# Kernel tuning notes

Hardware: AMD Instinct MI355X
Metric: run time of the kernel (lower is better)

Reference implementation:

```python
import jax, jax.numpy as jnp
import numpy as np

B, S, HID = 4, 2048, 576
NH, NKV, HD = 9, 3, 64
MAXPOS, THETA = 8192, 100000.0


def rotate_half(x):
    x1, x2 = x[..., : x.shape[-1] // 2], x[..., x.shape[-1] // 2 :]
    return jnp.concatenate((-x2, x1), axis=-1)


def setup_inputs() -> dict:
    key = jax.random.key(0)
    ks = jax.random.split(key, 6)
    x = jax.random.normal(ks[0], (B, S, HID), dtype=jnp.float32)
    # RoPE tables (HuggingFace layout: freqs duplicated across halves)
    inv_freq = 1.0 / (THETA ** (np.arange(0, HD, 2, dtype=np.float32) / HD))
    freqs = np.outer(np.arange(MAXPOS, dtype=np.float32), inv_freq)
    emb = np.concatenate([freqs, freqs], axis=-1)
    cos = jnp.asarray(np.cos(emb))
    sin = jnp.asarray(np.sin(emb))
    position_ids = jnp.broadcast_to(jnp.arange(S, dtype=jnp.int64), (B, S))
    # additive causal mask [B,1,S,S]
    causal = jnp.where(
        jnp.tril(jnp.ones((S, S), dtype=bool)), 0.0, -1e9
    ).astype(jnp.float32)
    attention_mask = jnp.broadcast_to(causal, (B, 1, S, S))
    scale = 0.02
    wq = jax.random.normal(ks[1], (NH * HD, HID), dtype=jnp.float32) * scale
    wk = jax.random.normal(ks[2], (NKV * HD, HID), dtype=jnp.float32) * scale
    wv = jax.random.normal(ks[3], (NKV * HD, HID), dtype=jnp.float32) * scale
    wo = jax.random.normal(ks[4], (HID, NH * HD), dtype=jnp.float32) * scale
    return {
        "x": x, "cos": cos, "sin": sin, "position_ids": position_ids,
        "attention_mask": attention_mask,
        "wq": wq, "wk": wk, "wv": wv, "wo": wo,
    }


def reference(x, cos, sin, position_ids, attention_mask, wq, wk, wv, wo):
    b, s, _ = x.shape
    # projections (nn.Linear: y = x @ W.T), split into heads -> [B,H,S,D]
    q = (x @ wq.T).reshape(b, s, NH, HD).transpose(0, 2, 1, 3)
    k = (x @ wk.T).reshape(b, s, NKV, HD).transpose(0, 2, 1, 3)
    v = (x @ wv.T).reshape(b, s, NKV, HD).transpose(0, 2, 1, 3)
    # RoPE: cos/sin gathered per position -> [B,1,S,D], broadcast over heads
    c = cos[position_ids][:, None, :, :]
    si = sin[position_ids][:, None, :, :]
    q = q * c + rotate_half(q) * si
    k = k * c + rotate_half(k) * si
    # GQA expansion: repeat_interleave kv heads to match q heads
    k = jnp.repeat(k, NH // NKV, axis=1)
    v = jnp.repeat(v, NH // NKV, axis=1)
    scale = 1.0 / jnp.sqrt(jnp.asarray(HD, dtype=x.dtype))
    scores = jnp.einsum("bhqd,bhkd->bhqk", q, k) * scale + attention_mask
    attn = jax.nn.softmax(scores.astype(jnp.float32), axis=-1).astype(q.dtype)
    out = jnp.einsum("bhqk,bhkd->bhqd", attn, v)
    out = out.transpose(0, 2, 1, 3).reshape(b, s, NH * HD)
    return out @ wo.T
```

## Files before the change

### kernel.cpp

```cpp
#include <hip/hip_runtime.h>
#include <hip/hip_bf16.h>

#define B_    4
#define S_    2048
#define HID_  576
#define NH_   9
#define NKV_  3
#define HD_   64
#define GQ_   3

typedef __attribute__((ext_vector_type(8))) short bf16x8;
typedef __attribute__((ext_vector_type(4))) float f32x4;

__device__ __forceinline__ short f2bf(float f) {
    union { float f; unsigned int u; } v; v.f = f;
    unsigned int r = (v.u + 0x7fffu + ((v.u >> 16) & 1u)) >> 16;
    return (short)r;
}

__device__ __forceinline__ float exp2fast(float x) {
    return __builtin_amdgcn_exp2f(x);
}

__device__ __forceinline__ void async16(const void* g, void* l) {
    __builtin_amdgcn_global_load_lds(
        (const __attribute__((address_space(1))) unsigned int*)g,
        (__attribute__((address_space(3))) unsigned int*)l, 16, 0, 0);
}

#define NX_   (8192 * 576)
#define NWQ_  (576 * 576)
#define NWK_  (192 * 576)
#define NWV_  (192 * 576)
#define NWO_  (576 * 576)
#define NTOT_ (NX_ + NWQ_ + NWK_ + NWV_ + NWO_)

__global__ __launch_bounds__(256) void convert_kernel(
    const float* __restrict__ x,  const float* __restrict__ wq,
    const float* __restrict__ wk, const float* __restrict__ wv,
    const float* __restrict__ wo,
    short* __restrict__ xb, short* __restrict__ wqkvb, short* __restrict__ wob)
{
    int i4 = (blockIdx.x * 256 + threadIdx.x) * 4;
    const float* src; short* dst;
    if (i4 < NX_)                          { src = x  + i4;                          dst = xb    + i4; }
    else if (i4 < NX_ + NWQ_)              { src = wq + (i4 - NX_);                  dst = wqkvb + (i4 - NX_); }
    else if (i4 < NX_ + NWQ_ + NWK_)       { src = wk + (i4 - NX_ - NWQ_);           dst = wqkvb + (i4 - NX_); }
    else if (i4 < NX_ + NWQ_ + NWK_ + NWV_){ src = wv + (i4 - NX_ - NWQ_ - NWK_);    dst = wqkvb + (i4 - NX_); }
    else                                   { src = wo + (i4 - NX_ - NWQ_ - NWK_ - NWV_);
                                             dst = wob + (i4 - NX_ - NWQ_ - NWK_ - NWV_); }
    float4 v = *(const float4*)src;
    short4 o = make_short4(f2bf(v.x), f2bf(v.y), f2bf(v.z), f2bf(v.w));
    *(short4*)dst = o;
}

__global__ __launch_bounds__(256) void qkv_kernel(
    const short* __restrict__ xb,
    const short* __restrict__ wqkvb,
    const float* __restrict__ cosb,
    const float* __restrict__ sinb,
    short* __restrict__ Q,
    short* __restrict__ K,
    short* __restrict__ Vt)
{
    __shared__ __align__(16) short As[2][256 * 64];
    __shared__ __align__(16) short Bs[2][64 * 64];

    const int m0     = blockIdx.x * 256;
    const int nb_blk = blockIdx.y;
    const int tid  = threadIdx.x;
    const int w    = tid >> 6, lane = tid & 63;
    const int quad = lane >> 4, c = lane & 15;
    const int lr   = lane >> 3, lg = lane & 7;
    const int sw   = lg ^ lr;
    const int xg   = quad ^ (c & 7);

    auto stage = [&](int step, short* dstA, short* dstB) {
        const int k0 = step * 64;
        #pragma unroll
        for (int r = 0; r < 8; ++r) {
            int ch = w * 8 + r, R = ch * 8 + lr;
            async16(xb + (size_t)(m0 + R) * HID_ + k0 + sw * 8, (char*)dstA + ch * 1024);
        }
        #pragma unroll
        for (int r = 0; r < 2; ++r) {
            int ch = w * 2 + r, R = ch * 8 + lr;
            async16(wqkvb + (size_t)(nb_blk * 64 + R) * HID_ + k0 + sw * 8, (char*)dstB + ch * 1024);
        }
    };

    f32x4 acc[4][4];
    #pragma unroll
    for (int mt = 0; mt < 4; ++mt)
        #pragma unroll
        for (int nb = 0; nb < 4; ++nb) acc[mt][nb] = (f32x4){0.f, 0.f, 0.f, 0.f};

    stage(0, As[0], Bs[0]);

    int buf = 0;
    for (int kk = 0; kk < 9; ++kk) {
        __syncthreads();
        if (kk < 8) stage(kk + 1, As[buf ^ 1], Bs[buf ^ 1]);

        const short* a_s = As[buf];
        const short* b_s = Bs[buf];
        bf16x8 bfr[4][2];
        #pragma unroll
        for (int nb = 0; nb < 4; ++nb) {
            int row = nb * 16 + c;
            bfr[nb][0] = *(const bf16x8*)(b_s + row * 64 + xg * 8);
            bfr[nb][1] = *(const bf16x8*)(b_s + row * 64 + (xg ^ 4) * 8);
        }
        #pragma unroll
        for (int mt = 0; mt < 4; ++mt) {
            int row = w * 64 + mt * 16 + c;
            bf16x8 a0 = *(const bf16x8*)(a_s + row * 64 + xg * 8);
            bf16x8 a1 = *(const bf16x8*)(a_s + row * 64 + (xg ^ 4) * 8);
            #pragma unroll
            for (int nb = 0; nb < 4; ++nb) {
                acc[mt][nb] = __builtin_amdgcn_mfma_f32_16x16x32_bf16(a0, bfr[nb][0], acc[mt][nb], 0, 0, 0);
                acc[mt][nb] = __builtin_amdgcn_mfma_f32_16x16x32_bf16(a1, bfr[nb][1], acc[mt][nb], 0, 0, 0);
            }
        }
        buf ^= 1;
    }

    int type, head;
    if (nb_blk < NH_)            { type = 0; head = nb_blk; }
    else if (nb_blk < NH_ + NKV_){ type = 1; head = nb_blk - NH_; }
    else                         { type = 2; head = nb_blk - NH_ - NKV_; }
    const int b  = m0 >> 11;
    const int s0 = m0 & (S_ - 1);

    if (type < 2) {
        const float qs = (type == 0) ? 0.18033688f : 1.0f;
        #pragma unroll
        for (int mt = 0; mt < 4; ++mt)
            #pragma unroll
            for (int reg = 0; reg < 4; ++reg) {
                int s = s0 + w * 64 + mt * 16 + quad * 4 + reg;
                const float* cr = cosb + (size_t)s * HD_;
                const float* sr = sinb + (size_t)s * HD_;
                float a0 = acc[mt][0][reg], a1 = acc[mt][1][reg];
                float a2 = acc[mt][2][reg], a3 = acc[mt][3][reg];
                float o0 = (a0 * cr[c]      - a2 * sr[c])      * qs;
                float o1 = (a1 * cr[c + 16] - a3 * sr[c + 16]) * qs;
                float o2 = (a2 * cr[c + 32] + a0 * sr[c + 32]) * qs;
                float o3 = (a3 * cr[c + 48] + a1 * sr[c + 48]) * qs;
                short* dst = (type == 0)
                    ? Q + (((size_t)b * NH_  + head) * S_ + s) * HD_
                    : K + (((size_t)b * NKV_ + head) * S_ + s) * HD_;
                dst[c]      = f2bf(o0);
                dst[c + 16] = f2bf(o1);
                dst[c + 32] = f2bf(o2);
                dst[c + 48] = f2bf(o3);
            }
    } else {
        short* base = Vt + (((size_t)b * NKV_ + head) * HD_) * S_;
        #pragma unroll
        for (int mt = 0; mt < 4; ++mt) {
            int s4 = s0 + w * 64 + mt * 16 + quad * 4;
            #pragma unroll
            for (int nb = 0; nb < 4; ++nb) {
                int d = nb * 16 + c;
                short4 pk = make_short4(f2bf(acc[mt][nb][0]), f2bf(acc[mt][nb][1]),
                                        f2bf(acc[mt][nb][2]), f2bf(acc[mt][nb][3]));
                *(short4*)(base + (size_t)d * S_ + s4) = pk;
            }
        }
    }
}

#define PSTR 72

__global__ __launch_bounds__(256) void attn_kernel(
    const short* __restrict__ Q,
    const short* __restrict__ K,
    const short* __restrict__ Vt,
    short* __restrict__ AOb)
{
    __shared__ __align__(16) short Qs[64 * 64];
    __shared__ __align__(16) short Ks[2][64 * 64];
    __shared__ __align__(16) short Vs[2][64 * 64];
    __shared__ __align__(16) short Ps[64 * PSTR];

    const int hb = blockIdx.x;
    const int h  = hb >> 2, b = hb & 3;
    const int qt = 31 - blockIdx.y;
    const int kh = h / GQ_;
    const int tid  = threadIdx.x;
    const int w    = tid >> 6, lane = tid & 63;
    const int quad = lane >> 4, c = lane & 15;
    const int lr   = lane >> 3, lg = lane & 7;
    const int sw   = lg ^ lr;
    const int xg   = quad ^ (c & 7);

    const short* Qg = Q  + (((size_t)b * NH_  + h ) * S_ + qt * 64) * HD_;
    const short* Kg = K  + (((size_t)b * NKV_ + kh) * S_) * HD_;
    const short* Vg = Vt + (((size_t)b * NKV_ + kh) * HD_) * S_;

    #pragma unroll
    for (int r = 0; r < 2; ++r) {
        int ch = w * 2 + r, R = ch * 8 + lr;
        async16(Qg + (size_t)R * HD_ + sw * 8, (char*)Qs + ch * 1024);
    }
    #pragma unroll
    for (int r = 0; r < 4; ++r) {
        int it = w * 4 + r;
        if (it < 8) {
            int R = it * 8 + lr;
            async16(Kg + (size_t)R * HD_ + sw * 8, (char*)Ks[0] + it * 1024);
        } else {
            int R = (it - 8) * 8 + lr;
            async16(Vg + (size_t)R * S_ + sw * 8, (char*)Vs[0] + (it - 8) * 1024);
        }
    }

    bf16x8 ones;
    #pragma unroll
    for (int i = 0; i < 8; ++i) ones[i] = (short)0x3F80;

    f32x4 acc_o[4];
    #pragma unroll
    for (int nb = 0; nb < 4; ++nb) acc_o[nb] = (f32x4){0.f, 0.f, 0.f, 0.f};
    f32x4 acc_l = (f32x4){0.f, 0.f, 0.f, 0.f};

    bf16x8 aq0, aq1;

    auto do_tile = [&](const short* ks, const short* vs, bool MASK) {
        f32x4 sc[4];
        #pragma unroll
        for (int nb = 0; nb < 4; ++nb) {
            bf16x8 bk0 = *(const bf16x8*)(ks + (nb * 16 + c) * 64 + xg * 8);
            bf16x8 bk1 = *(const bf16x8*)(ks + (nb * 16 + c) * 64 + (xg ^ 4) * 8);
            f32x4 z = (f32x4){0.f, 0.f, 0.f, 0.f};
            z = __builtin_amdgcn_mfma_f32_16x16x32_bf16(aq0, bk0, z, 0, 0, 0);
            z = __builtin_amdgcn_mfma_f32_16x16x32_bf16(aq1, bk1, z, 0, 0, 0);
            sc[nb] = z;
        }
        #pragma unroll
        for (int r = 0; r < 4; ++r) {
            const int qrow = w * 16 + quad * 4 + r;
            #pragma unroll
            for (int nb = 0; nb < 4; ++nb) {
                float sv = sc[nb][r] - 4.0f;
                if (MASK && (nb * 16 + c > qrow)) sv = -1e30f;
                Ps[(w * 16 + quad * 4 + r) * PSTR + nb * 16 + c] = f2bf(exp2fast(sv));
            }
        }
        #pragma unroll
        for (int kc = 0; kc < 2; ++kc) {
            bf16x8 ap = *(const bf16x8*)(Ps + (w * 16 + c) * PSTR + quad * 8 + kc * 32);
            int pg = kc ? (xg ^ 4) : xg;
            #pragma unroll
            for (int nb = 0; nb < 4; ++nb) {
                bf16x8 bv = *(const bf16x8*)(vs + (nb * 16 + c) * 64 + pg * 8);
                acc_o[nb] = __builtin_amdgcn_mfma_f32_16x16x32_bf16(ap, bv, acc_o[nb], 0, 0, 0);
            }
            acc_l = __builtin_amdgcn_mfma_f32_16x16x32_bf16(ap, ones, acc_l, 0, 0, 0);
        }
    };

    __syncthreads();
    aq0 = *(const bf16x8*)(Qs + (w * 16 + c) * 64 + xg * 8);
    aq1 = *(const bf16x8*)(Qs + (w * 16 + c) * 64 + (xg ^ 4) * 8);

    int buf = 0;
    for (int kt = 0; kt < qt; ++kt) {
        int nxt = buf ^ 1;
        #pragma unroll
        for (int r = 0; r < 4; ++r) {
            int it = w * 4 + r;
            if (it < 8) {
                int R = it * 8 + lr;
                async16(Kg + (size_t)((kt + 1) * 64 + R) * HD_ + sw * 8,
                        (char*)Ks[nxt] + it * 1024);
            } else {
                int R = (it - 8) * 8 + lr;
                async16(Vg + (size_t)R * S_ + (kt + 1) * 64 + sw * 8,
                        (char*)Vs[nxt] + (it - 8) * 1024);
            }
        }
        do_tile(Ks[buf], Vs[buf], false);
        __syncthreads();
        buf ^= 1;
    }
    do_tile(Ks[buf], Vs[buf], true);

    #pragma unroll
    for (int r = 0; r < 4; ++r) {
        int s = qt * 64 + w * 16 + quad * 4 + r;
        float inv = 1.f / acc_l[r];
        short* dst = AOb + (((size_t)b * S_ + s) * NH_ + h) * HD_;
        #pragma unroll
        for (int nb = 0; nb < 4; ++nb)
            dst[nb * 16 + c] = f2bf(acc_o[nb][r] * inv);
    }
}

__global__ __launch_bounds__(256) void oproj_kernel(
    const short* __restrict__ AOb,
    const short* __restrict__ wob,
    float* __restrict__ out)
{
    __shared__ __align__(16) short As[2][256 * 64];
    __shared__ __align__(16) short Bs[2][64 * 64];

    const int m0 = blockIdx.x * 256;
    const int n0 = blockIdx.y * 64;
    const int tid  = threadIdx.x;
    const int w    = tid >> 6, lane = tid & 63;
    const int quad = lane >> 4, c = lane & 15;
    const int lr   = lane >> 3, lg = lane & 7;
    const int sw   = lg ^ lr;
    const int xg   = quad ^ (c & 7);

    auto stage = [&](int step, short* dstA, short* dstB) {
        const int k0 = step * 64;
        #pragma unroll
        for (int r = 0; r < 8; ++r) {
            int ch = w * 8 + r, R = ch * 8 + lr;
            async16(AOb + (size_t)(m0 + R) * HID_ + k0 + sw * 8, (char*)dstA + ch * 1024);
        }
        #pragma unroll
        for (int r = 0; r < 2; ++r) {
            int ch = w * 2 + r, R = ch * 8 + lr;
            async16(wob + (size_t)(n0 + R) * HID_ + k0 + sw * 8, (char*)dstB + ch * 1024);
        }
    };

    f32x4 acc[4][4];
    #pragma unroll
    for (int mt = 0; mt < 4; ++mt)
        #pragma unroll
        for (int nb = 0; nb < 4; ++nb) acc[mt][nb] = (f32x4){0.f, 0.f, 0.f, 0.f};

    stage(0, As[0], Bs[0]);

    int buf = 0;
    for (int kk = 0; kk < 9; ++kk) {
        __syncthreads();
        if (kk < 8) stage(kk + 1, As[buf ^ 1], Bs[buf ^ 1]);

        const short* a_s = As[buf];
        const short* b_s = Bs[buf];
        bf16x8 bfr[4][2];
        #pragma unroll
        for (int nb = 0; nb < 4; ++nb) {
            int row = nb * 16 + c;
            bfr[nb][0] = *(const bf16x8*)(b_s + row * 64 + xg * 8);
            bfr[nb][1] = *(const bf16x8*)(b_s + row * 64 + (xg ^ 4) * 8);
        }
        #pragma unroll
        for (int mt = 0; mt < 4; ++mt) {
            int row = w * 64 + mt * 16 + c;
            bf16x8 a0 = *(const bf16x8*)(a_s + row * 64 + xg * 8);
            bf16x8 a1 = *(const bf16x8*)(a_s + row * 64 + (xg ^ 4) * 8);
            #pragma unroll
            for (int nb = 0; nb < 4; ++nb) {
                acc[mt][nb] = __builtin_amdgcn_mfma_f32_16x16x32_bf16(a0, bfr[nb][0], acc[mt][nb], 0, 0, 0);
                acc[mt][nb] = __builtin_amdgcn_mfma_f32_16x16x32_bf16(a1, bfr[nb][1], acc[mt][nb], 0, 0, 0);
            }
        }
        buf ^= 1;
    }

    #pragma unroll
    for (int mt = 0; mt < 4; ++mt)
        #pragma unroll
        for (int reg = 0; reg < 4; ++reg) {
            int m = m0 + w * 64 + mt * 16 + quad * 4 + reg;
            float* dst = out + (size_t)m * HID_ + n0;
            #pragma unroll
            for (int nb = 0; nb < 4; ++nb)
                dst[nb * 16 + c] = acc[mt][nb][reg];
        }
}

extern "C" void kernel_launch(void* const* d_in, const int* in_sizes, int n_in,
                              void* d_out, int out_size, void* d_ws, size_t ws_size,
                              hipStream_t stream) {
    const float* x    = (const float*)d_in[0];
    const float* cosb = (const float*)d_in[1];
    const float* sinb = (const float*)d_in[2];
    const float* wq   = (const float*)d_in[5];
    const float* wk   = (const float*)d_in[6];
    const float* wv   = (const float*)d_in[7];
    const float* wo   = (const float*)d_in[8];

    short* xb    = (short*)d_ws;
    short* wqkvb = xb    + (size_t)NX_;
    short* wob   = wqkvb + (size_t)(NWQ_ + NWK_ + NWV_);
    short* Qb    = wob   + (size_t)NWO_;
    short* Kb    = Qb    + (size_t)B_ * NH_  * S_ * HD_;
    short* Vtb   = Kb    + (size_t)B_ * NKV_ * S_ * HD_;
    short* AOb   = Vtb   + (size_t)B_ * NKV_ * S_ * HD_;

    convert_kernel<<<dim3(NTOT_ / 4 / 256), dim3(256), 0, stream>>>(
        x, wq, wk, wv, wo, xb, wqkvb, wob);
    qkv_kernel<<<dim3(32, 15), dim3(256), 0, stream>>>(
        xb, wqkvb, cosb, sinb, Qb, Kb, Vtb);
    attn_kernel<<<dim3(36, 32), dim3(256), 0, stream>>>(Qb, Kb, Vtb, AOb);
    oproj_kernel<<<dim3(32, 9), dim3(256), 0, stream>>>(AOb, wob, (float*)d_out);
}
```

Baseline: 191.7 us.

## Restructure attention P staging, load Q directly to registers, swizzle GEMM block order

The attention kernel now swaps the MFMA operands so each lane holds scores along keys. This lets P be written to a smaller LDS buffer in two halves with packed bf16 converts, and the PV MFMAs are interleaved with the exp work. Q is loaded straight from global memory into registers instead of going through LDS, and the K/V staging addressing is simplified into precomputed pointers with per-wave roles. The QKV and output-projection GEMMs use a 1D grid remapped so consecutive blocks land on different XCDs, for better L2 locality. These changes together aim to cut LDS traffic, conversion instructions and cache misses, at the cost of more register pressure and an unswizzled global Q read.

Measured after the change: 192.7 us. Within noise of the previous version (+0.5%).

```diff
diff --git a/kernel.cpp b/kernel.cpp
--- a/kernel.cpp
+++ b/kernel.cpp
@@ -16,6 +16,12 @@
     union { float f; unsigned int u; } v; v.f = f;
     unsigned int r = (v.u + 0x7fffu + ((v.u >> 16) & 1u)) >> 16;
     return (short)r;
+}
+
+__device__ __forceinline__ unsigned int cvt_pk_bf16(float a, float b) {
+    unsigned int r;
+    asm("v_cvt_pk_bf16_f32 %0, %1, %2" : "=v"(r) : "v"(a), "v"(b));
+    return r;
 }
 
 __device__ __forceinline__ float exp2fast(float x) {
@@ -66,8 +72,10 @@
     __shared__ __align__(16) short As[2][256 * 64];
     __shared__ __align__(16) short Bs[2][64 * 64];
 
-    const int m0     = blockIdx.x * 256;
-    const int nb_blk = blockIdx.y;
+    const int bid = blockIdx.x;
+    const int f   = (bid & 7) * 60 + (bid >> 3);
+    const int m0     = (f / 15) * 256;
+    const int nb_blk = f % 15;
     const int tid  = threadIdx.x;
     const int w    = tid >> 6, lane = tid & 63;
     const int quad = lane >> 4, c = lane & 15;
@@ -171,7 +179,7 @@
     }
 }
 
-#define PSTR 72
+#define PSH 40
 
 __global__ __launch_bounds__(256) void attn_kernel(
     const short* __restrict__ Q,
@@ -179,10 +187,9 @@
     const short* __restrict__ Vt,
     short* __restrict__ AOb)
 {
-    __shared__ __align__(16) short Qs[64 * 64];
     __shared__ __align__(16) short Ks[2][64 * 64];
     __shared__ __align__(16) short Vs[2][64 * 64];
-    __shared__ __align__(16) short Ps[64 * PSTR];
+    __shared__ __align__(16) short Ps[64 * PSH];
 
     const int hb = blockIdx.x;
     const int h  = hb >> 2, b = hb & 3;
@@ -199,22 +206,23 @@
     const short* Kg = K  + (((size_t)b * NKV_ + kh) * S_) * HD_;
     const short* Vg = Vt + (((size_t)b * NKV_ + kh) * HD_) * S_;
 
-    #pragma unroll
-    for (int r = 0; r < 2; ++r) {
-        int ch = w * 2 + r, R = ch * 8 + lr;
-        async16(Qg + (size_t)R * HD_ + sw * 8, (char*)Qs + ch * 1024);
-    }
+    bf16x8 aq0 = *(const bf16x8*)(Qg + (w * 16 + c) * HD_ + quad * 8);
+    bf16x8 aq1 = *(const bf16x8*)(Qg + (w * 16 + c) * HD_ + 32 + quad * 8);
+
+    const bool stK = (w < 2);
+    const int  ch0 = (w & 1) * 4;
+    const short* gs[4];
     #pragma unroll
     for (int r = 0; r < 4; ++r) {
-        int it = w * 4 + r;
-        if (it < 8) {
-            int R = it * 8 + lr;
-            async16(Kg + (size_t)R * HD_ + sw * 8, (char*)Ks[0] + it * 1024);
-        } else {
-            int R = (it - 8) * 8 + lr;
-            async16(Vg + (size_t)R * S_ + sw * 8, (char*)Vs[0] + (it - 8) * 1024);
-        }
-    }
+        int ch = ch0 + r;
+        gs[r] = stK ? Kg + (size_t)(ch * 8 + lr) * HD_ + sw * 8
+                    : Vg + (size_t)(ch * 8 + lr) * S_  + sw * 8;
+    }
+    const int gstep = stK ? 64 * HD_ : 64;
+
+    #pragma unroll
+    for (int r = 0; r < 4; ++r)
+        async16(gs[r], (char*)(stK ? Ks[0] : Vs[0]) + (ch0 + r) * 1024);
 
     bf16x8 ones;
     #pragma unroll
@@ -224,8 +232,6 @@
     #pragma unroll
     for (int nb = 0; nb < 4; ++nb) acc_o[nb] = (f32x4){0.f, 0.f, 0.f, 0.f};
     f32x4 acc_l = (f32x4){0.f, 0.f, 0.f, 0.f};
-
-    bf16x8 aq0, aq1;
 
     auto do_tile = [&](const short* ks, const short* vs, bool MASK) {
         f32x4 sc[4];
@@ -234,52 +240,46 @@
             bf16x8 bk0 = *(const bf16x8*)(ks + (nb * 16 + c) * 64 + xg * 8);
             bf16x8 bk1 = *(const bf16x8*)(ks + (nb * 16 + c) * 64 + (xg ^ 4) * 8);
             f32x4 z = (f32x4){0.f, 0.f, 0.f, 0.f};
-            z = __builtin_amdgcn_mfma_f32_16x16x32_bf16(aq0, bk0, z, 0, 0, 0);
-            z = __builtin_amdgcn_mfma_f32_16x16x32_bf16(aq1, bk1, z, 0, 0, 0);
+            z = __builtin_amdgcn_mfma_f32_16x16x32_bf16(bk0, aq0, z, 0, 0, 0);
+            z = __builtin_amdgcn_mfma_f32_16x16x32_bf16(bk1, aq1, z, 0, 0, 0);
             sc[nb] = z;
         }
         #pragma unroll
-        for (int r = 0; r < 4; ++r) {
-            const int qrow = w * 16 + quad * 4 + r;
-            #pragma unroll
-            for (int nb = 0; nb < 4; ++nb) {
-                float sv = sc[nb][r] - 4.0f;
-                if (MASK && (nb * 16 + c > qrow)) sv = -1e30f;
-                Ps[(w * 16 + quad * 4 + r) * PSTR + nb * 16 + c] = f2bf(exp2fast(sv));
-            }
-        }
-        #pragma unroll
-        for (int kc = 0; kc < 2; ++kc) {
-            bf16x8 ap = *(const bf16x8*)(Ps + (w * 16 + c) * PSTR + quad * 8 + kc * 32);
-            int pg = kc ? (xg ^ 4) : xg;
-            #pragma unroll
-            for (int nb = 0; nb < 4; ++nb) {
-                bf16x8 bv = *(const bf16x8*)(vs + (nb * 16 + c) * 64 + pg * 8);
-                acc_o[nb] = __builtin_amdgcn_mfma_f32_16x16x32_bf16(ap, bv, acc_o[nb], 0, 0, 0);
+        for (int ph = 0; ph < 2; ++ph) {
+            #pragma unroll
+            for (int nbh = 0; nbh < 2; ++nbh) {
+                const int nb = ph * 2 + nbh;
+                float p[4];
+                #pragma unroll
+                for (int r = 0; r < 4; ++r) {
+                    float pv = exp2fast(sc[nb][r] - 4.0f);
+                    if (MASK && (nb * 16 + quad * 4 + r > w * 16 + c)) pv = 0.f;
+                    p[r] = pv;
+                }
+                uint2 t;
+                t.x = cvt_pk_bf16(p[0], p[1]);
+                t.y = cvt_pk_bf16(p[2], p[3]);
+                *(uint2*)(Ps + (w * 16 + c) * PSH + nbh * 16 + quad * 4) = t;
+            }
+            bf16x8 ap = *(const bf16x8*)(Ps + (w * 16 + c) * PSH + quad * 8);
+            const int pg = ph ? (xg ^ 4) : xg;
+            #pragma unroll
+            for (int nb2 = 0; nb2 < 4; ++nb2) {
+                bf16x8 bv = *(const bf16x8*)(vs + (nb2 * 16 + c) * 64 + pg * 8);
+                acc_o[nb2] = __builtin_amdgcn_mfma_f32_16x16x32_bf16(ap, bv, acc_o[nb2], 0, 0, 0);
             }
             acc_l = __builtin_amdgcn_mfma_f32_16x16x32_bf16(ap, ones, acc_l, 0, 0, 0);
         }
     };
 
     __syncthreads();
-    aq0 = *(const bf16x8*)(Qs + (w * 16 + c) * 64 + xg * 8);
-    aq1 = *(const bf16x8*)(Qs + (w * 16 + c) * 64 + (xg ^ 4) * 8);
-
     int buf = 0;
     for (int kt = 0; kt < qt; ++kt) {
         int nxt = buf ^ 1;
         #pragma unroll
         for (int r = 0; r < 4; ++r) {
-            int it = w * 4 + r;
-            if (it < 8) {
-                int R = it * 8 + lr;
-                async16(Kg + (size_t)((kt + 1) * 64 + R) * HD_ + sw * 8,
-                        (char*)Ks[nxt] + it * 1024);
-            } else {
-                int R = (it - 8) * 8 + lr;
-                async16(Vg + (size_t)R * S_ + (kt + 1) * 64 + sw * 8,
-                        (char*)Vs[nxt] + (it - 8) * 1024);
-            }
+            gs[r] += gstep;
+            async16(gs[r], (char*)(stK ? Ks[nxt] : Vs[nxt]) + (ch0 + r) * 1024);
         }
         do_tile(Ks[buf], Vs[buf], false);
         __syncthreads();
@@ -306,8 +306,10 @@
     __shared__ __align__(16) short As[2][256 * 64];
     __shared__ __align__(16) short Bs[2][64 * 64];
 
-    const int m0 = blockIdx.x * 256;
-    const int n0 = blockIdx.y * 64;
+    const int bid = blockIdx.x;
+    const int f   = (bid & 7) * 36 + (bid >> 3);
+    const int m0 = (f / 9) * 256;
+    const int n0 = (f % 9) * 64;
     const int tid  = threadIdx.x;
     const int w    = tid >> 6, lane = tid & 63;
     const int quad = lane >> 4, c = lane & 15;
@@ -398,8 +400,8 @@
 
     convert_kernel<<<dim3(NTOT_ / 4 / 256), dim3(256), 0, stream>>>(
         x, wq, wk, wv, wo, xb, wqkvb, wob);
-    qkv_kernel<<<dim3(32, 15), dim3(256), 0, stream>>>(
+    qkv_kernel<<<dim3(480), dim3(256), 0, stream>>>(
         xb, wqkvb, cosb, sinb, Qb, Kb, Vtb);
     attn_kernel<<<dim3(36, 32), dim3(256), 0, stream>>>(Qb, Kb, Vtb, AOb);
-    oproj_kernel<<<dim3(32, 9), dim3(256), 0, stream>>>(AOb, wob, (float*)d_out);
-}
+    oproj_kernel<<<dim3(288), dim3(256), 0, stream>>>(AOb, wob, (float*)d_out);
+}
```
